# Kernel optimization log

Measured on AMD Instinct MI355X. Metric: run time of the kernel, lower is better.

The kernel has to match this reference:

```python
import jax, jax.numpy as jnp
import numpy as np

B = 262144          # number of graphs
TOTAL_N = 33554432  # total nodes = B * mean_size(128)


def _make_sizes():
    rng = np.random.default_rng(0)
    sizes = rng.integers(64, 193, size=B).astype(np.int64)  # mean 128
    d = int(TOTAL_N - sizes.sum())
    if d != 0:
        sizes[: abs(d)] += 1 if d > 0 else -1  # min size 64, so -1 is safe
    assert int(sizes.sum()) == TOTAL_N
    return sizes


def setup_inputs() -> dict:
    key = jax.random.key(0)
    sizes = _make_sizes()
    x = jax.random.normal(key, (TOTAL_N,), dtype=jnp.float32)
    return {"x": x, "graph_size_list": jnp.asarray(sizes, dtype=jnp.int64)}


def reference(x, graph_size_list):
    # Per ragged segment, emit a one-hot vector at the argmax position
    # (torch.argmax returns the FIRST maximal index; replicate that tie-break).
    N = x.shape[0]
    nB = graph_size_list.shape[0]
    seg = jnp.repeat(jnp.arange(nB), graph_size_list, total_repeat_length=N)  # [N]
    seg_max = jax.ops.segment_max(x, seg, num_segments=nB)                    # [B]
    pos = jnp.arange(N)
    # candidate global index where x hits its segment max; N (sentinel) elsewhere
    cand = jnp.where(x == seg_max[seg], pos, N)
    first = jax.ops.segment_min(cand, seg, num_segments=nB)                   # [B]
    one = jnp.ones((), dtype=x.dtype)
    return jnp.zeros((N,), dtype=x.dtype).at[first].set(one)
```

## Files before the change

### kernel.cpp

```cpp
#include <hip/hip_runtime.h>
#include <limits.h>


__global__ void scan_stage1(const int* __restrict__ sizes,
                            int* __restrict__ offs,
                            int* __restrict__ blocksums, int B) {
    int tid = threadIdx.x;
    int gid = blockIdx.x * 256 + tid;
    int v = (gid < B) ? sizes[gid] : 0;
    int lane = tid & 63;
    int incl = v;
    #pragma unroll
    for (int off = 1; off < 64; off <<= 1) {
        int n = __shfl_up(incl, off, 64);
        if (lane >= off) incl += n;
    }
    __shared__ int wsum[4];
    if (lane == 63) wsum[tid >> 6] = incl;
    __syncthreads();
    int base = 0;
    int wv = tid >> 6;
    for (int i = 0; i < wv; ++i) base += wsum[i];
    if (gid < B) offs[gid] = base + incl - v;
    if (tid == 255) blocksums[blockIdx.x] = base + incl;
}

__global__ void scan_stage2(int* __restrict__ blocksums, int nb) {
    int tid = threadIdx.x;
    int v = (tid < nb) ? blocksums[tid] : 0;
    int lane = tid & 63;
    int incl = v;
    #pragma unroll
    for (int off = 1; off < 64; off <<= 1) {
        int n = __shfl_up(incl, off, 64);
        if (lane >= off) incl += n;
    }
    __shared__ int wsum[16];
    if (lane == 63) wsum[tid >> 6] = incl;
    __syncthreads();
    int base = 0;
    int wv = tid >> 6;
    for (int i = 0; i < wv; ++i) base += wsum[i];
    if (tid < nb) blocksums[tid] = base + incl - v;
}

__global__ __launch_bounds__(256) void zero_fill(float4* __restrict__ out4, int n4) {
    int stride = gridDim.x * blockDim.x;
    float4 z = make_float4(0.f, 0.f, 0.f, 0.f);
    for (int i = blockIdx.x * blockDim.x + threadIdx.x; i < n4; i += stride)
        out4[i] = z;
}

__global__ __launch_bounds__(256) void argmax_scatter(
        const float* __restrict__ x,
        const int* __restrict__ sizes,
        const int* __restrict__ offs,
        const int* __restrict__ blockoffs,
        float* __restrict__ out, int B) {
    int s = blockIdx.x * 256 + threadIdx.x;
    if (s >= B) return;
    int start = offs[s] + blockoffs[s >> 8];
    int size  = sizes[s];
    const float* p = x + start;

    float best = -__builtin_inff();
    int   bi   = 0;

    int h = (4 - (start & 3)) & 3;
    if (h > size) h = size;
    int i = 0;
    for (; i < h; ++i) {
        float v = p[i];
        if (v > best) { best = v; bi = i; }
    }
    int n4 = (size - i) >> 2;
    const float4* p4 = reinterpret_cast<const float4*>(p + i);
    #pragma unroll 4
    for (int j = 0; j < n4; ++j) {
        float4 v = p4[j];
        int b = i + 4 * j;
        if (v.x > best) { best = v.x; bi = b;     }
        if (v.y > best) { best = v.y; bi = b + 1; }
        if (v.z > best) { best = v.z; bi = b + 2; }
        if (v.w > best) { best = v.w; bi = b + 3; }
    }
    i += n4 << 2;
    for (; i < size; ++i) {
        float v = p[i];
        if (v > best) { best = v; bi = i; }
    }
    out[start + bi] = 1.0f;
}

extern "C" void kernel_launch(void* const* d_in, const int* in_sizes, int n_in,
                              void* d_out, int out_size, void* d_ws, size_t ws_size,
                              hipStream_t stream) {
    const float* x     = (const float*)d_in[0];
    const int*   sizes = (const int*)d_in[1];
    float*       out   = (float*)d_out;
    int B = in_sizes[1];
    int N = in_sizes[0];

    int* offs      = (int*)d_ws;
    int* blocksums = offs + B;

    int nb1 = (B + 255) / 256;
    scan_stage1<<<nb1, 256, 0, stream>>>(sizes, offs, blocksums, B);
    scan_stage2<<<1, 1024, 0, stream>>>(blocksums, nb1);

    zero_fill<<<2048, 256, 0, stream>>>((float4*)out, N / 4);
    int ab = (B + 255) / 256;
    argmax_scatter<<<ab, 256, 0, stream>>>(x, sizes, offs, blocksums, out, B);
}
```

Measured before the change: 281.1 us.

## Fuse zero-fill and argmax into block-per-64-segments LDS-staged kernel

Replaces the separate zero-fill kernel and the one-thread-per-segment argmax with a single kernel. Each block stages the contiguous span of 64 segments into swizzled shared memory with coalesced float4 loads, computes the argmax with 4 threads per segment plus shuffle reductions, and writes the one-hot output for that span with coalesced stores. This removes the extra full pass over the output and the uncoalesced per-thread strided reads. In exchange it uses about 48KB of LDS per block, which limits occupancy, and relies on 64 segments always fitting in the LDS buffer (at most 64*192 floats).

```diff
diff --git a/kernel.cpp b/kernel.cpp
--- a/kernel.cpp
+++ b/kernel.cpp
@@ -1,6 +1,8 @@
 #include <hip/hip_runtime.h>
 #include <limits.h>
 
+
+#define SW(w) ((w) ^ ((((w) >> 7) & 7) << 2))
 
 __global__ void scan_stage1(const int* __restrict__ sizes,
                             int* __restrict__ offs,
@@ -44,52 +46,85 @@
     if (tid < nb) blocksums[tid] = base + incl - v;
 }
 
-__global__ __launch_bounds__(256) void zero_fill(float4* __restrict__ out4, int n4) {
-    int stride = gridDim.x * blockDim.x;
-    float4 z = make_float4(0.f, 0.f, 0.f, 0.f);
-    for (int i = blockIdx.x * blockDim.x + threadIdx.x; i < n4; i += stride)
-        out4[i] = z;
-}
-
-__global__ __launch_bounds__(256) void argmax_scatter(
+__global__ __launch_bounds__(256) void seg_onehot(
         const float* __restrict__ x,
         const int* __restrict__ sizes,
         const int* __restrict__ offs,
         const int* __restrict__ blockoffs,
         float* __restrict__ out, int B) {
-    int s = blockIdx.x * 256 + threadIdx.x;
-    if (s >= B) return;
-    int start = offs[s] + blockoffs[s >> 8];
-    int size  = sizes[s];
-    const float* p = x + start;
+    __shared__ float lds[12384];
+    const int t  = threadIdx.x;
+    const int s0 = blockIdx.x * 64;
+    if (s0 >= B) return;
+    const int lastSeg = (s0 + 63 < B) ? s0 + 63 : B - 1;
 
+    const int bo     = blockoffs[s0 >> 8];
+    const int s_abs  = offs[s0] + bo;
+    const int e_abs  = offs[lastSeg] + bo + sizes[lastSeg];
+    const int gbase  = s_abs & ~3;
+    const int nw4    = (e_abs - gbase + 3) >> 2;
+
+    const float4* __restrict__ x4 = reinterpret_cast<const float4*>(x + gbase);
+    for (int j = t; j < nw4; j += 256) {
+        float4 v = x4[j];
+        int w = j << 2;
+        *reinterpret_cast<float4*>(&lds[SW(w)]) = v;
+    }
+    __syncthreads();
+
+    const int seg = s0 + (t >> 2);
+    const int q   = t & 3;
     float best = -__builtin_inff();
-    int   bi   = 0;
+    int   bi   = INT_MAX;
+    int   lstart = 0;
+    if (seg < B) {
+        lstart = offs[seg] + bo - gbase;
+        const int size = sizes[seg];
+        for (int i = q; i < size; i += 4) {
+            int w = lstart + i;
+            float v = lds[SW(w)];
+            if (v > best) { best = v; bi = i; }
+        }
+    }
+    #pragma unroll
+    for (int off = 1; off <= 2; off <<= 1) {
+        float ov = __shfl_xor(best, off, 64);
+        int   oi = __shfl_xor(bi, off, 64);
+        if (ov > best || (ov == best && oi < bi)) { best = ov; bi = oi; }
+    }
+    __syncthreads();
 
-    int h = (4 - (start & 3)) & 3;
-    if (h > size) h = size;
-    int i = 0;
-    for (; i < h; ++i) {
-        float v = p[i];
-        if (v > best) { best = v; bi = i; }
+    const float4 z = make_float4(0.f, 0.f, 0.f, 0.f);
+    for (int j = t; j < nw4; j += 256) {
+        int w = j << 2;
+        *reinterpret_cast<float4*>(&lds[SW(w)]) = z;
     }
-    int n4 = (size - i) >> 2;
-    const float4* p4 = reinterpret_cast<const float4*>(p + i);
-    #pragma unroll 4
-    for (int j = 0; j < n4; ++j) {
-        float4 v = p4[j];
-        int b = i + 4 * j;
-        if (v.x > best) { best = v.x; bi = b;     }
-        if (v.y > best) { best = v.y; bi = b + 1; }
-        if (v.z > best) { best = v.z; bi = b + 2; }
-        if (v.w > best) { best = v.w; bi = b + 3; }
+    __syncthreads();
+    if (q == 0 && seg < B) {
+        int w = lstart + bi;
+        lds[SW(w)] = 1.0f;
     }
-    i += n4 << 2;
-    for (; i < size; ++i) {
-        float v = p[i];
-        if (v > best) { best = v; bi = i; }
+    __syncthreads();
+
+    const int a4 = (s_abs + 3) & ~3;
+    const int e4 = e_abs & ~3;
+    const int nh = a4 - s_abs;
+    if (t < nh) {
+        int w = s_abs - gbase + t;
+        out[s_abs + t] = lds[SW(w)];
     }
-    out[start + bi] = 1.0f;
+    float4* __restrict__ out4 = reinterpret_cast<float4*>(out + a4);
+    const int nb4 = (e4 - a4) >> 2;
+    const int wb  = a4 - gbase;
+    for (int j = t; j < nb4; j += 256) {
+        int w = wb + (j << 2);
+        out4[j] = *reinterpret_cast<const float4*>(&lds[SW(w)]);
+    }
+    const int nt = e_abs - e4;
+    if (t < nt) {
+        int w = e4 - gbase + t;
+        out[e4 + t] = lds[SW(w)];
+    }
 }
 
 extern "C" void kernel_launch(void* const* d_in, const int* in_sizes, int n_in,
@@ -99,7 +134,6 @@
     const int*   sizes = (const int*)d_in[1];
     float*       out   = (float*)d_out;
     int B = in_sizes[1];
-    int N = in_sizes[0];
 
     int* offs      = (int*)d_ws;
     int* blocksums = offs + B;
@@ -108,7 +142,6 @@
     scan_stage1<<<nb1, 256, 0, stream>>>(sizes, offs, blocksums, B);
     scan_stage2<<<1, 1024, 0, stream>>>(blocksums, nb1);
 
-    zero_fill<<<2048, 256, 0, stream>>>((float4*)out, N / 4);
-    int ab = (B + 255) / 256;
-    argmax_scatter<<<ab, 256, 0, stream>>>(x, sizes, offs, blocksums, out, B);
+    int blocks = (B + 63) / 64;
+    seg_onehot<<<blocks, 256, 0, stream>>>(x, sizes, offs, blocksums, out, B);
 }
```

After: 264.8 us. 5.8% less time.

## Fuse zero-fill into block-cooperative segmented argmax using shared-memory atomicMax keys

Applied to the files above, without the earlier changes.

Replaces the one-thread-per-segment argmax and the separate zero-fill kernel with a single kernel. Each 256-thread block handles 64 consecutive segments and reads their span with coalesced float4 loads. It zeroes the output in the same pass and reduces per-segment argmax through 64-bit packed (ordered value, inverted index) keys with shared-memory atomicMax. This removes the uncoalesced per-thread strided reads and one full output pass, at the cost of a per-element binary search over segment starts and shared atomics. The key packing keeps the first-index tie-break.

```diff
diff --git a/kernel.cpp b/kernel.cpp
--- a/kernel.cpp
+++ b/kernel.cpp
@@ -1,5 +1,4 @@
 #include <hip/hip_runtime.h>
-#include <limits.h>
 
 
 __global__ void scan_stage1(const int* __restrict__ sizes,
@@ -44,52 +43,83 @@
     if (tid < nb) blocksums[tid] = base + incl - v;
 }
 
-__global__ __launch_bounds__(256) void zero_fill(float4* __restrict__ out4, int n4) {
-    int stride = gridDim.x * blockDim.x;
-    float4 z = make_float4(0.f, 0.f, 0.f, 0.f);
-    for (int i = blockIdx.x * blockDim.x + threadIdx.x; i < n4; i += stride)
-        out4[i] = z;
-}
-
-__global__ __launch_bounds__(256) void argmax_scatter(
+__global__ __launch_bounds__(256) void seg_atomic_onehot(
         const float* __restrict__ x,
         const int* __restrict__ sizes,
         const int* __restrict__ offs,
         const int* __restrict__ blockoffs,
         float* __restrict__ out, int B) {
-    int s = blockIdx.x * 256 + threadIdx.x;
-    if (s >= B) return;
-    int start = offs[s] + blockoffs[s >> 8];
-    int size  = sizes[s];
-    const float* p = x + start;
+    __shared__ int sstart[65];
+    __shared__ unsigned long long skey[64];
+    const int t  = threadIdx.x;
+    const int s0 = blockIdx.x * 64;
+    if (s0 >= B) return;
+    const int nseg = (s0 + 64 <= B) ? 64 : (B - s0);
+    const int bo   = blockoffs[s0 >> 8];
+    if (t < nseg) {
+        sstart[t] = offs[s0 + t] + bo;
+        skey[t]   = 0ULL;
+    }
+    if (t == 0) {
+        const int last = s0 + nseg - 1;
+        sstart[nseg] = offs[last] + bo + sizes[last];
+    }
+    __syncthreads();
+    const int s_abs = sstart[0];
+    const int e_abs = sstart[nseg];
+    const int gbase = s_abs & ~3;
+    const int nw4   = (e_abs - gbase + 3) >> 2;
+    const float4* __restrict__ x4 = reinterpret_cast<const float4*>(x + gbase);
+    const float4 z4 = make_float4(0.f, 0.f, 0.f, 0.f);
 
-    float best = -__builtin_inff();
-    int   bi   = 0;
+    for (int j = t; j < nw4; j += 256) {
+        const float4 v = x4[j];
+        const int g0 = gbase + (j << 2);
 
-    int h = (4 - (start & 3)) & 3;
-    if (h > size) h = size;
-    int i = 0;
-    for (; i < h; ++i) {
-        float v = p[i];
-        if (v > best) { best = v; bi = i; }
+        if (g0 >= s_abs && g0 + 4 <= e_abs) {
+            *reinterpret_cast<float4*>(out + g0) = z4;
+        } else {
+            #pragma unroll
+            for (int e = 0; e < 4; ++e) {
+                const int gi = g0 + e;
+                if (gi >= s_abs && gi < e_abs) out[gi] = 0.0f;
+            }
+        }
+
+        int lo = 0;
+        #pragma unroll
+        for (int step = 32; step >= 1; step >>= 1) {
+            const int cand = lo + step;
+            if (cand < nseg && sstart[cand] <= g0) lo = cand;
+        }
+        const int cur = sstart[lo];
+        const int nxt = sstart[lo + 1];
+
+        unsigned long long kA = 0ULL, kB = 0ULL;
+        const float vv[4] = {v.x, v.y, v.z, v.w};
+        #pragma unroll
+        for (int e = 0; e < 4; ++e) {
+            const int gi = g0 + e;
+            if (gi < s_abs || gi >= e_abs) continue;
+            unsigned u = __float_as_uint(vv[e]);
+            u = ((int)u < 0) ? ~u : (u | 0x80000000u);
+            const bool inB = (gi >= nxt);
+            const int  sb  = inB ? nxt : cur;
+            const unsigned long long k =
+                ((unsigned long long)u << 32) | (0xFFFFFFFFu - (unsigned)(gi - sb));
+            if (inB) { if (k > kB) kB = k; }
+            else     { if (k > kA) kA = k; }
+        }
+        if (kA) atomicMax(&skey[lo], kA);
+        if (kB) atomicMax(&skey[lo + 1], kB);
     }
-    int n4 = (size - i) >> 2;
-    const float4* p4 = reinterpret_cast<const float4*>(p + i);
-    #pragma unroll 4
-    for (int j = 0; j < n4; ++j) {
-        float4 v = p4[j];
-        int b = i + 4 * j;
-        if (v.x > best) { best = v.x; bi = b;     }
-        if (v.y > best) { best = v.y; bi = b + 1; }
-        if (v.z > best) { best = v.z; bi = b + 2; }
-        if (v.w > best) { best = v.w; bi = b + 3; }
+    __syncthreads();
+
+    if (t < nseg) {
+        const unsigned long long k = skey[t];
+        const int li = (int)(0xFFFFFFFFu - (unsigned)(k & 0xFFFFFFFFull));
+        out[sstart[t] + li] = 1.0f;
     }
-    i += n4 << 2;
-    for (; i < size; ++i) {
-        float v = p[i];
-        if (v > best) { best = v; bi = i; }
-    }
-    out[start + bi] = 1.0f;
 }
 
 extern "C" void kernel_launch(void* const* d_in, const int* in_sizes, int n_in,
@@ -99,7 +129,6 @@
     const int*   sizes = (const int*)d_in[1];
     float*       out   = (float*)d_out;
     int B = in_sizes[1];
-    int N = in_sizes[0];
 
     int* offs      = (int*)d_ws;
     int* blocksums = offs + B;
@@ -108,7 +137,6 @@
     scan_stage1<<<nb1, 256, 0, stream>>>(sizes, offs, blocksums, B);
     scan_stage2<<<1, 1024, 0, stream>>>(blocksums, nb1);
 
-    zero_fill<<<2048, 256, 0, stream>>>((float4*)out, N / 4);
-    int ab = (B + 255) / 256;
-    argmax_scatter<<<ab, 256, 0, stream>>>(x, sizes, offs, blocksums, out, B);
+    int blocks = (B + 63) / 64;
+    seg_atomic_onehot<<<blocks, 256, 0, stream>>>(x, sizes, offs, blocksums, out, B);
 }
```

Result: faster. 266.3 us (-5.3%).

## Use 16 threads per segment and fuse zero-fill into one-hot writes

Applied to the files above, without the earlier changes.

Replaces the one-thread-per-segment argmax with 16 lanes cooperating on each segment, using coalesced float4 loads and a shuffle reduction with first-index tie-break. The separate zero_fill kernel is removed: each segment writes its own full output slice, zeros plus the one-hot entry. This aims to fix the uncoalesced, serial per-thread scans and to drop one kernel launch and a separate output pass. The cost is extra shuffle work and divergent handling of the head and tail elements.

```diff
diff --git a/kernel.cpp b/kernel.cpp
--- a/kernel.cpp
+++ b/kernel.cpp
@@ -44,52 +44,62 @@
     if (tid < nb) blocksums[tid] = base + incl - v;
 }
 
-__global__ __launch_bounds__(256) void zero_fill(float4* __restrict__ out4, int n4) {
-    int stride = gridDim.x * blockDim.x;
-    float4 z = make_float4(0.f, 0.f, 0.f, 0.f);
-    for (int i = blockIdx.x * blockDim.x + threadIdx.x; i < n4; i += stride)
-        out4[i] = z;
-}
-
-__global__ __launch_bounds__(256) void argmax_scatter(
+__global__ __launch_bounds__(256) void seg16_onehot(
         const float* __restrict__ x,
         const int* __restrict__ sizes,
         const int* __restrict__ offs,
         const int* __restrict__ blockoffs,
         float* __restrict__ out, int B) {
-    int s = blockIdx.x * 256 + threadIdx.x;
+    const int t = threadIdx.x;
+    const int g = t >> 4;
+    const int r = t & 15;
+    const int s = blockIdx.x * 16 + g;
     if (s >= B) return;
-    int start = offs[s] + blockoffs[s >> 8];
-    int size  = sizes[s];
-    const float* p = x + start;
-
-    float best = -__builtin_inff();
-    int   bi   = 0;
+    const int bo    = blockoffs[blockIdx.x >> 4];
+    const int start = offs[s] + bo;
+    const int size  = sizes[s];
 
     int h = (4 - (start & 3)) & 3;
     if (h > size) h = size;
-    int i = 0;
-    for (; i < h; ++i) {
-        float v = p[i];
-        if (v > best) { best = v; bi = i; }
+    const int m4 = (size - h) >> 2;
+    const int tl = size - h - (m4 << 2);
+
+    float best = -__builtin_inff();
+    int   bi   = INT_MAX;
+    #define UPD(vv, ii) do { float _v = (vv); int _i = (ii); \
+        if (_v > best || (_v == best && _i < bi)) { best = _v; bi = _i; } } while (0)
+
+    if (r < h) UPD(x[start + r], r);
+    const float4* __restrict__ p4 = reinterpret_cast<const float4*>(x + start + h);
+    #pragma unroll 3
+    for (int k = r; k < m4; k += 16) {
+        const float4 v = p4[k];
+        const int li = h + (k << 2);
+        UPD(v.x, li); UPD(v.y, li + 1); UPD(v.z, li + 2); UPD(v.w, li + 3);
     }
-    int n4 = (size - i) >> 2;
-    const float4* p4 = reinterpret_cast<const float4*>(p + i);
-    #pragma unroll 4
-    for (int j = 0; j < n4; ++j) {
-        float4 v = p4[j];
-        int b = i + 4 * j;
-        if (v.x > best) { best = v.x; bi = b;     }
-        if (v.y > best) { best = v.y; bi = b + 1; }
-        if (v.z > best) { best = v.z; bi = b + 2; }
-        if (v.w > best) { best = v.w; bi = b + 3; }
+    if (r < tl) { const int li = h + (m4 << 2) + r; UPD(x[start + li], li); }
+    #undef UPD
+
+    #pragma unroll
+    for (int m = 1; m <= 8; m <<= 1) {
+        const float ov = __shfl_xor(best, m, 64);
+        const int   oi = __shfl_xor(bi, m, 64);
+        if (ov > best || (ov == best && oi < bi)) { best = ov; bi = oi; }
     }
-    i += n4 << 2;
-    for (; i < size; ++i) {
-        float v = p[i];
-        if (v > best) { best = v; bi = i; }
+
+    if (r < h) out[start + r] = (r == bi) ? 1.0f : 0.0f;
+    float4* __restrict__ o4 = reinterpret_cast<float4*>(out + start + h);
+    #pragma unroll 3
+    for (int k = r; k < m4; k += 16) {
+        const int li = h + (k << 2);
+        float4 o;
+        o.x = (li     == bi) ? 1.0f : 0.0f;
+        o.y = (li + 1 == bi) ? 1.0f : 0.0f;
+        o.z = (li + 2 == bi) ? 1.0f : 0.0f;
+        o.w = (li + 3 == bi) ? 1.0f : 0.0f;
+        o4[k] = o;
     }
-    out[start + bi] = 1.0f;
+    if (r < tl) { const int li = h + (m4 << 2) + r; out[start + li] = (li == bi) ? 1.0f : 0.0f; }
 }
 
 extern "C" void kernel_launch(void* const* d_in, const int* in_sizes, int n_in,
@@ -99,7 +109,6 @@
     const int*   sizes = (const int*)d_in[1];
     float*       out   = (float*)d_out;
     int B = in_sizes[1];
-    int N = in_sizes[0];
 
     int* offs      = (int*)d_ws;
     int* blocksums = offs + B;
@@ -108,7 +117,6 @@
     scan_stage1<<<nb1, 256, 0, stream>>>(sizes, offs, blocksums, B);
     scan_stage2<<<1, 1024, 0, stream>>>(blocksums, nb1);
 
-    zero_fill<<<2048, 256, 0, stream>>>((float4*)out, N / 4);
-    int ab = (B + 255) / 256;
-    argmax_scatter<<<ab, 256, 0, stream>>>(x, sizes, offs, blocksums, out, B);
+    int blocks = (B + 15) / 16;
+    seg16_onehot<<<blocks, 256, 0, stream>>>(x, sizes, offs, blocksums, out, B);
 }
```

New measurement: 250.3 us. -10.9%, faster.
